# Optimization experiments

Hardware: AMD Instinct MI355X
Metric: run time of the kernel (lower is better)

## Reference

```python
import jax, jax.numpy as jnp
import numpy as np

DEPTH, FEAT, HID = 20, 2048, 1024
HALF = FEAT // 2
CLAMP = 2.0
TWO_OVER_PI = 0.6366197723675814  # FrEIA's 0.636619772


def setup_inputs() -> dict:
    key = jax.random.key(0)
    ks = jax.random.split(key, 9)
    x = jax.random.normal(ks[0], (4096, FEAT), dtype=jnp.float32)
    # FrEIA PermuteRandom: numpy permutation seeded with layer index k
    perms = jnp.asarray(
        np.stack([np.random.RandomState(k).permutation(FEAT) for k in range(DEPTH)]),
        dtype=jnp.int32,
    )
    def w(k, shape):  # module reinits all params as 0.01*randn
        return 0.01 * jax.random.normal(k, shape, dtype=jnp.float32)
    return {
        "x": x, "perms": perms,
        "s1_w1": w(ks[1], (DEPTH, HALF, HID)), "s1_b1": w(ks[2], (DEPTH, HID)),
        "s1_w2": w(ks[3], (DEPTH, HID, FEAT)), "s1_b2": w(ks[4], (DEPTH, FEAT)),
        "s2_w1": w(ks[5], (DEPTH, HALF, HID)), "s2_b1": w(ks[6], (DEPTH, HID)),
        "s2_w2": w(ks[7], (DEPTH, HID, FEAT)), "s2_b2": w(ks[8], (DEPTH, FEAT)),
    }


def _subnet(x, w1, b1, w2, b2):
    h = x @ w1 + b1
    h = jnp.where(h >= 0, h, 0.01 * h)  # LeakyReLU(negative_slope=0.01)
    return h @ w2 + b2


def reference(x, perms, s1_w1, s1_b1, s1_w2, s1_b2, s2_w1, s2_b1, s2_w2, s2_b2):
    def body(carry, xs):
        z, jac = carry
        perm, w1a, b1a, w1b, b1b, w2a, b2a, w2b, b2b = xs
        z = z[:, perm]                       # PermuteRandom
        x1, x2 = z[:, :HALF], z[:, HALF:]    # GLOW coupling split
        r2 = _subnet(x2, w2a, b2a, w2b, b2b)  # [B, FEAT] -> (s2, t2)
        e2 = CLAMP * TWO_OVER_PI * jnp.arctan(r2[:, :HALF] / CLAMP)
        y1 = jnp.exp(e2) * x1 + r2[:, HALF:]
        r1 = _subnet(y1, w1a, b1a, w1b, b1b)  # (s1, t1)
        e1 = CLAMP * TWO_OVER_PI * jnp.arctan(r1[:, :HALF] / CLAMP)
        y2 = jnp.exp(e1) * x2 + r1[:, HALF:]
        jac = jac + e1.sum(-1) + e2.sum(-1)  # log|det J| per sample
        return (jnp.concatenate([y1, y2], axis=-1), jac), None

    jac0 = jnp.zeros(x.shape[0], dtype=x.dtype)
    (z, jac), _ = jax.lax.scan(
        body, (x, jac0),
        (perms, s1_w1, s1_b1, s1_w2, s1_b2, s2_w1, s2_b1, s2_w2, s2_b2),
    )
    return z, jac
```

## Files before the change

### kernel.cpp

```cpp
#include <hip/hip_runtime.h>
#include <stdint.h>

#define DEPTH 20
#define FEAT  2048
#define HALF  1024
#define HID   1024
#define MROWS 4096

typedef __bf16 bf16x8 __attribute__((ext_vector_type(8)));
typedef float  f32x4  __attribute__((ext_vector_type(4)));
typedef unsigned int u32x4 __attribute__((ext_vector_type(4)));

__device__ __forceinline__ unsigned short f2bf(float f) {
  union { float f; unsigned int u; } v; v.f = f;
  unsigned int u = v.u + 0x7fffu + ((v.u >> 16) & 1u);
  return (unsigned short)(u >> 16);
}

__device__ __forceinline__ void async_cp16(unsigned short* lds, const unsigned short* g) {
  __builtin_amdgcn_global_load_lds(
      (const __attribute__((address_space(1))) void*)g,
      (__attribute__((address_space(3))) void*)lds, 16, 0, 0);
}

__device__ __forceinline__ bf16x8 lds_ld8(const unsigned short* p) {
  return __builtin_bit_cast(bf16x8, *(const u32x4*)p);
}

__global__ void wcvt_k(const float* __restrict__ s2w1, const float* __restrict__ s2w2,
                       const float* __restrict__ s1w1, const float* __restrict__ s1w2,
                       unsigned short* __restrict__ w2a, unsigned short* __restrict__ w2b,
                       unsigned short* __restrict__ w1a, unsigned short* __restrict__ w1b) {
  const int zid = blockIdx.z;
  const int d = zid >> 2, which = zid & 3;
  const float* src; unsigned short* dst; int N, pp;
  switch (which) {
    case 0:  src = s2w1 + (size_t)d * HALF * HID;  dst = w2a + (size_t)d * HALF * HID; N = 1024; pp = 0; break;
    case 1:  src = s2w2 + (size_t)d * HID * FEAT;  dst = w2b + (size_t)d * FEAT * HID; N = 2048; pp = 1; break;
    case 2:  src = s1w1 + (size_t)d * HALF * HID;  dst = w1a + (size_t)d * HALF * HID; N = 1024; pp = 0; break;
    default: src = s1w2 + (size_t)d * HID * FEAT;  dst = w1b + (size_t)d * FEAT * HID; N = 2048; pp = 1; break;
  }
  int nb = blockIdx.x * 32;
  if (nb >= N) return;
  int kb = blockIdx.y * 32;
  __shared__ float t[32][33];
  int tx = threadIdx.x, ty = threadIdx.y;
#pragma unroll
  for (int s = 0; s < 4; ++s)
    t[ty + 8*s][tx] = src[(size_t)(kb + ty + 8*s) * N + nb + tx];
  __syncthreads();
  int pbase = pp ? (nb < 1024 ? 2*nb : 2*(nb - 1024) + 32) : nb;
#pragma unroll
  for (int s = 0; s < 4; ++s) {
    int nl = ty + 8*s;
    dst[(size_t)(pbase + nl) * 1024 + kb + tx] = f2bf(t[tx][nl]);
  }
}

__device__ __forceinline__ int porig(int p) {
  int g = p >> 6, o = p & 63;
  return (o < 32) ? (g*32 + o) : (1024 + g*32 + (o - 32));
}

__global__ void bias_k(const float* __restrict__ s2b1, const float* __restrict__ s2b2,
                       const float* __restrict__ s1b1, const float* __restrict__ s1b2,
                       float* __restrict__ b2a, float* __restrict__ b2b,
                       float* __restrict__ b1a, float* __restrict__ b1b) {
  int i = blockIdx.x * 256 + threadIdx.x;
  if (i >= DEPTH * 6144) return;
  int d = i / 6144, j = i - d * 6144;
  if (j < 1024)      b2a[d*1024 + j] = s2b1[(size_t)d*HID + j];
  else if (j < 3072) { int p = j - 1024; b2b[d*2048 + p] = s2b2[(size_t)d*FEAT + porig(p)]; }
  else if (j < 4096) b1a[d*1024 + j - 3072] = s1b1[(size_t)d*HID + j - 3072];
  else               { int p = j - 4096; b1b[d*2048 + p] = s1b2[(size_t)d*FEAT + porig(p)]; }
}

__global__ void permute_k(const float* __restrict__ z, const int* __restrict__ perm,
                          float* __restrict__ x1f, float* __restrict__ x2f,
                          unsigned short* __restrict__ x2b) {
  int c = blockIdx.x * 256 + threadIdx.x;
  int row0 = blockIdx.y * 8;
  int pc = perm[c];
#pragma unroll
  for (int r = 0; r < 8; ++r) {
    int row = row0 + r;
    float v = z[row * FEAT + pc];
    if (c < HALF) {
      x1f[row * HALF + c] = v;
    } else {
      x2f[row * HALF + c - HALF] = v;
      x2b[row * HALF + c - HALF] = f2bf(v);
    }
  }
}

template<int EPI>
__launch_bounds__(256)
__global__ void gemm_k(const unsigned short* __restrict__ A,
                       const unsigned short* __restrict__ Bt,
                       const float* __restrict__ bias,
                       const float* __restrict__ xin,
                       float* __restrict__ yout,
                       unsigned short* __restrict__ ybf,
                       float* __restrict__ jac,
                       unsigned short* __restrict__ hout) {
  __shared__ unsigned short As[2][128 * 32];
  __shared__ unsigned short Bs[2][128 * 32];
  const int tid  = threadIdx.x;
  const int wave = tid >> 6, lane = tid & 63;
  const int quad = lane >> 4, l15 = lane & 15;
  const int wy = wave >> 1, wx = wave & 1;
  const int bm = blockIdx.y * 128;
  const int bn = blockIdx.x * 128;
  const int K = 1024;

  f32x4 acc[4][4];
#pragma unroll
  for (int i = 0; i < 4; ++i)
#pragma unroll
    for (int j = 0; j < 4; ++j)
#pragma unroll
      for (int r = 0; r < 4; ++r) acc[i][j][r] = 0.0f;

  const int gbase = wave * 64 + lane;

  auto stage = [&](int kt, int buf) {
    const int k0 = kt * 32;
#pragma unroll
    for (int i = 0; i < 2; ++i) {
      int g  = i * 256 + gbase;
      int r  = g >> 2, kg = g & 3;
      async_cp16(&As[buf][(i * 256 + wave * 64) * 8], A  + (size_t)(bm + r) * K + k0 + kg * 8);
      async_cp16(&Bs[buf][(i * 256 + wave * 64) * 8], Bt + (size_t)(bn + r) * K + k0 + kg * 8);
    }
  };

  stage(0, 0);
  __syncthreads();

  for (int kt = 0; kt < 32; ++kt) {
    const int cur = kt & 1;
    if (kt < 31) stage(kt + 1, cur ^ 1);

    bf16x8 af[4], bf[4];
#pragma unroll
    for (int i = 0; i < 4; ++i)
      af[i] = lds_ld8(&As[cur][(wy * 64 + i * 16 + l15) * 32 + quad * 8]);
#pragma unroll
    for (int j = 0; j < 4; ++j)
      bf[j] = lds_ld8(&Bs[cur][(wx * 64 + j * 16 + l15) * 32 + quad * 8]);
#pragma unroll
    for (int i = 0; i < 4; ++i)
#pragma unroll
      for (int j = 0; j < 4; ++j)
        acc[i][j] = __builtin_amdgcn_mfma_f32_16x16x32_bf16(af[i], bf[j], acc[i][j], 0, 0, 0);

    __syncthreads();
  }

  if (EPI == 0) {
    const int ldo = gridDim.x * 128;
#pragma unroll
    for (int j = 0; j < 4; ++j) {
      int col = bn + wx * 64 + j * 16 + l15;
      float bj = bias[col];
#pragma unroll
      for (int i = 0; i < 4; ++i) {
#pragma unroll
        for (int r = 0; r < 4; ++r) {
          int row = bm + wy * 64 + i * 16 + quad * 4 + r;
          float v = acc[i][j][r] + bj;
          v = v >= 0.0f ? v : 0.01f * v;
          hout[(size_t)row * ldo + col] = f2bf(v);
        }
      }
    }
  } else {
    const int g = (bn >> 6) + wx;
#pragma unroll
    for (int i = 0; i < 4; ++i) {
      float esum[4] = {0.0f, 0.0f, 0.0f, 0.0f};
#pragma unroll
      for (int j = 0; j < 2; ++j) {
        int pe = bn + wx * 64 + j * 16 + l15;
        float be = bias[pe];
        float ba = bias[pe + 32];
        int xcol = g * 32 + j * 16 + l15;
#pragma unroll
        for (int r = 0; r < 4; ++r) {
          int row = bm + wy * 64 + i * 16 + quad * 4 + r;
          float re = acc[i][j][r] + be;
          float ra = acc[i][j + 2][r] + ba;
          float e  = 1.2732395447351628f * atanf(0.5f * re);
          float y  = __expf(e) * xin[(size_t)row * HALF + xcol] + ra;
          yout[(size_t)row * FEAT + xcol] = y;
          if (ybf) ybf[(size_t)row * HALF + xcol] = f2bf(y);
          esum[r] += e;
        }
      }
#pragma unroll
      for (int r = 0; r < 4; ++r) {
        float v = esum[r];
        v += __shfl_xor(v, 1);
        v += __shfl_xor(v, 2);
        v += __shfl_xor(v, 4);
        v += __shfl_xor(v, 8);
        if (l15 == 0) {
          int row = bm + wy * 64 + i * 16 + quad * 4 + r;
          atomicAdd(&jac[row], v);
        }
      }
    }
  }
}

__global__ void jcopy_k(const float* __restrict__ jac, float* __restrict__ out) {
  int i = blockIdx.x * 256 + threadIdx.x;
  if (i < 4096) out[i] = jac[i];
}

extern "C" void kernel_launch(void* const* d_in, const int* in_sizes, int n_in,
                              void* d_out, int out_size, void* d_ws, size_t ws_size,
                              hipStream_t stream) {
  const float* x     = (const float*)d_in[0];
  const int*   perms = (const int*)d_in[1];
  const float* s1w1  = (const float*)d_in[2];
  const float* s1b1  = (const float*)d_in[3];
  const float* s1w2  = (const float*)d_in[4];
  const float* s1b2  = (const float*)d_in[5];
  const float* s2w1  = (const float*)d_in[6];
  const float* s2b1  = (const float*)d_in[7];
  const float* s2w2  = (const float*)d_in[8];
  const float* s2b2  = (const float*)d_in[9];
  float* out = (float*)d_out;

  size_t off = 0;
  char* base = (char*)d_ws;
  auto alloc = [&](size_t bytes) {
    void* r = base + off;
    off += (bytes + 255) & ~(size_t)255;
    return r;
  };
  float*          x1f = (float*)alloc((size_t)MROWS * HALF * 4);
  float*          x2f = (float*)alloc((size_t)MROWS * HALF * 4);
  unsigned short* x2b = (unsigned short*)alloc((size_t)MROWS * HALF * 2);
  unsigned short* y1b = (unsigned short*)alloc((size_t)MROWS * HALF * 2);
  unsigned short* hb  = (unsigned short*)alloc((size_t)MROWS * HID * 2);
  float*          zbuf= (float*)alloc((size_t)MROWS * FEAT * 4);
  unsigned short* w2a = (unsigned short*)alloc((size_t)DEPTH * HALF * HID * 2);
  unsigned short* w2b = (unsigned short*)alloc((size_t)DEPTH * FEAT * HID * 2);
  unsigned short* w1a = (unsigned short*)alloc((size_t)DEPTH * HALF * HID * 2);
  unsigned short* w1b = (unsigned short*)alloc((size_t)DEPTH * FEAT * HID * 2);
  float* b2a = (float*)alloc((size_t)DEPTH * 1024 * 4);
  float* b2b = (float*)alloc((size_t)DEPTH * 2048 * 4);
  float* b1a = (float*)alloc((size_t)DEPTH * 1024 * 4);
  float* b1b = (float*)alloc((size_t)DEPTH * 2048 * 4);
  float* jac = (float*)alloc(4096 * 4);

  hipMemsetAsync(jac, 0, 4096 * 4, stream);

  wcvt_k<<<dim3(64, 32, 4 * DEPTH), dim3(32, 8), 0, stream>>>(
      s2w1, s2w2, s1w1, s1w2, w2a, w2b, w1a, w1b);
  bias_k<<<(DEPTH * 6144 + 255) / 256, 256, 0, stream>>>(
      s2b1, s2b2, s1b1, s1b2, b2a, b2b, b1a, b1b);

  for (int d = 0; d < DEPTH; ++d) {
    const float* zsrc = (d == 0) ? x : zbuf;
    permute_k<<<dim3(8, 512), 256, 0, stream>>>(zsrc, perms + (size_t)d * FEAT, x1f, x2f, x2b);

    unsigned short* W2a = w2a + (size_t)d * HALF * HID;
    unsigned short* W2b = w2b + (size_t)d * FEAT * HID;
    unsigned short* W1a = w1a + (size_t)d * HALF * HID;
    unsigned short* W1b = w1b + (size_t)d * FEAT * HID;
    float* B2a = b2a + (size_t)d * 1024;
    float* B2b = b2b + (size_t)d * 2048;
    float* B1a = b1a + (size_t)d * 1024;
    float* B1b = b1b + (size_t)d * 2048;

    float* zdst = (d == DEPTH - 1) ? out : zbuf;
    gemm_k<0><<<dim3(8, 32), 256, 0, stream>>>(x2b, W2a, B2a, nullptr, nullptr, nullptr, nullptr, hb);
    gemm_k<1><<<dim3(16, 32), 256, 0, stream>>>(hb, W2b, B2b, x1f, zdst, y1b, jac, nullptr);
    gemm_k<0><<<dim3(8, 32), 256, 0, stream>>>(y1b, W1a, B1a, nullptr, nullptr, nullptr, nullptr, hb);
    gemm_k<1><<<dim3(16, 32), 256, 0, stream>>>(hb, W1b, B1b, x2f, zdst + HALF, nullptr, jac, nullptr);
  }
  jcopy_k<<<16, 256, 0, stream>>>(jac, out + (size_t)MROWS * FEAT);
}
```

Baseline: 4.355 ms.

## Shrink GEMM tile to 64x128, deepen K step to 64, add XOR-swizzled LDS

Changes the GEMM block tile from 128x128 to 64x128 and doubles the grid in M, giving twice as many workgroups on the 256-CU part. Each K step now covers 64 instead of 32. It uses a single LDS buffer with an explicit vmcnt wait instead of double buffering, and XOR-swizzles 16-byte chunks within a row to avoid LDS bank conflicts on the fragment reads. The trade-offs are lost global/compute overlap and lower reuse of B per block.

```diff
diff --git a/kernel.cpp b/kernel.cpp
--- a/kernel.cpp
+++ b/kernel.cpp
@@ -104,19 +104,19 @@
                        unsigned short* __restrict__ ybf,
                        float* __restrict__ jac,
                        unsigned short* __restrict__ hout) {
-  __shared__ unsigned short As[2][128 * 32];
-  __shared__ unsigned short Bs[2][128 * 32];
+  __shared__ unsigned short As[64 * 64];
+  __shared__ unsigned short Bs[128 * 64];
   const int tid  = threadIdx.x;
   const int wave = tid >> 6, lane = tid & 63;
   const int quad = lane >> 4, l15 = lane & 15;
   const int wy = wave >> 1, wx = wave & 1;
-  const int bm = blockIdx.y * 128;
+  const int bm = blockIdx.y * 64;
   const int bn = blockIdx.x * 128;
   const int K = 1024;
 
-  f32x4 acc[4][4];
-#pragma unroll
-  for (int i = 0; i < 4; ++i)
+  f32x4 acc[2][4];
+#pragma unroll
+  for (int i = 0; i < 2; ++i)
 #pragma unroll
     for (int j = 0; j < 4; ++j)
 #pragma unroll
@@ -124,37 +124,42 @@
 
   const int gbase = wave * 64 + lane;
 
-  auto stage = [&](int kt, int buf) {
-    const int k0 = kt * 32;
+  for (int kt = 0; kt < 16; ++kt) {
+    const int k0 = kt * 64;
 #pragma unroll
     for (int i = 0; i < 2; ++i) {
       int g  = i * 256 + gbase;
-      int r  = g >> 2, kg = g & 3;
-      async_cp16(&As[buf][(i * 256 + wave * 64) * 8], A  + (size_t)(bm + r) * K + k0 + kg * 8);
-      async_cp16(&Bs[buf][(i * 256 + wave * 64) * 8], Bt + (size_t)(bn + r) * K + k0 + kg * 8);
-    }
-  };
-
-  stage(0, 0);
-  __syncthreads();
-
-  for (int kt = 0; kt < 32; ++kt) {
-    const int cur = kt & 1;
-    if (kt < 31) stage(kt + 1, cur ^ 1);
-
-    bf16x8 af[4], bf[4];
-#pragma unroll
-    for (int i = 0; i < 4; ++i)
-      af[i] = lds_ld8(&As[cur][(wy * 64 + i * 16 + l15) * 32 + quad * 8]);
-#pragma unroll
-    for (int j = 0; j < 4; ++j)
-      bf[j] = lds_ld8(&Bs[cur][(wx * 64 + j * 16 + l15) * 32 + quad * 8]);
-#pragma unroll
-    for (int i = 0; i < 4; ++i)
-#pragma unroll
-      for (int j = 0; j < 4; ++j)
-        acc[i][j] = __builtin_amdgcn_mfma_f32_16x16x32_bf16(af[i], bf[j], acc[i][j], 0, 0, 0);
-
+      int r  = g >> 3, kg = (g & 7) ^ (r & 7);
+      async_cp16(&As[(i * 256 + wave * 64) * 8], A + (size_t)(bm + r) * K + k0 + kg * 8);
+    }
+#pragma unroll
+    for (int i = 0; i < 4; ++i) {
+      int g  = i * 256 + gbase;
+      int r  = g >> 3, kg = (g & 7) ^ (r & 7);
+      async_cp16(&Bs[(i * 256 + wave * 64) * 8], Bt + (size_t)(bn + r) * K + k0 + kg * 8);
+    }
+    asm volatile("s_waitcnt vmcnt(0)" ::: "memory");
+    __syncthreads();
+
+#pragma unroll
+    for (int kk = 0; kk < 2; ++kk) {
+      bf16x8 af[2], bf[4];
+#pragma unroll
+      for (int i = 0; i < 2; ++i) {
+        int ar = wy * 32 + i * 16 + l15;
+        af[i] = lds_ld8(&As[ar * 64 + (((kk * 4 + quad) ^ (ar & 7))) * 8]);
+      }
+#pragma unroll
+      for (int j = 0; j < 4; ++j) {
+        int br = wx * 64 + j * 16 + l15;
+        bf[j] = lds_ld8(&Bs[br * 64 + (((kk * 4 + quad) ^ (br & 7))) * 8]);
+      }
+#pragma unroll
+      for (int i = 0; i < 2; ++i)
+#pragma unroll
+        for (int j = 0; j < 4; ++j)
+          acc[i][j] = __builtin_amdgcn_mfma_f32_16x16x32_bf16(af[i], bf[j], acc[i][j], 0, 0, 0);
+    }
     __syncthreads();
   }
 
@@ -165,10 +170,10 @@
       int col = bn + wx * 64 + j * 16 + l15;
       float bj = bias[col];
 #pragma unroll
-      for (int i = 0; i < 4; ++i) {
+      for (int i = 0; i < 2; ++i) {
 #pragma unroll
         for (int r = 0; r < 4; ++r) {
-          int row = bm + wy * 64 + i * 16 + quad * 4 + r;
+          int row = bm + wy * 32 + i * 16 + quad * 4 + r;
           float v = acc[i][j][r] + bj;
           v = v >= 0.0f ? v : 0.01f * v;
           hout[(size_t)row * ldo + col] = f2bf(v);
@@ -178,7 +183,7 @@
   } else {
     const int g = (bn >> 6) + wx;
 #pragma unroll
-    for (int i = 0; i < 4; ++i) {
+    for (int i = 0; i < 2; ++i) {
       float esum[4] = {0.0f, 0.0f, 0.0f, 0.0f};
 #pragma unroll
       for (int j = 0; j < 2; ++j) {
@@ -188,7 +193,7 @@
         int xcol = g * 32 + j * 16 + l15;
 #pragma unroll
         for (int r = 0; r < 4; ++r) {
-          int row = bm + wy * 64 + i * 16 + quad * 4 + r;
+          int row = bm + wy * 32 + i * 16 + quad * 4 + r;
           float re = acc[i][j][r] + be;
           float ra = acc[i][j + 2][r] + ba;
           float e  = 1.2732395447351628f * atanf(0.5f * re);
@@ -206,7 +211,7 @@
         v += __shfl_xor(v, 4);
         v += __shfl_xor(v, 8);
         if (l15 == 0) {
-          int row = bm + wy * 64 + i * 16 + quad * 4 + r;
+          int row = bm + wy * 32 + i * 16 + quad * 4 + r;
           atomicAdd(&jac[row], v);
         }
       }
@@ -278,10 +283,10 @@
     float* B1b = b1b + (size_t)d * 2048;
 
     float* zdst = (d == DEPTH - 1) ? out : zbuf;
-    gemm_k<0><<<dim3(8, 32), 256, 0, stream>>>(x2b, W2a, B2a, nullptr, nullptr, nullptr, nullptr, hb);
-    gemm_k<1><<<dim3(16, 32), 256, 0, stream>>>(hb, W2b, B2b, x1f, zdst, y1b, jac, nullptr);
-    gemm_k<0><<<dim3(8, 32), 256, 0, stream>>>(y1b, W1a, B1a, nullptr, nullptr, nullptr, nullptr, hb);
-    gemm_k<1><<<dim3(16, 32), 256, 0, stream>>>(hb, W1b, B1b, x2f, zdst + HALF, nullptr, jac, nullptr);
+    gemm_k<0><<<dim3(8, 64), 256, 0, stream>>>(x2b, W2a, B2a, nullptr, nullptr, nullptr, nullptr, hb);
+    gemm_k<1><<<dim3(16, 64), 256, 0, stream>>>(hb, W2b, B2b, x1f, zdst, y1b, jac, nullptr);
+    gemm_k<0><<<dim3(8, 64), 256, 0, stream>>>(y1b, W1a, B1a, nullptr, nullptr, nullptr, nullptr, hb);
+    gemm_k<1><<<dim3(16, 64), 256, 0, stream>>>(hb, W1b, B1b, x2f, zdst + HALF, nullptr, jac, nullptr);
   }
   jcopy_k<<<16, 256, 0, stream>>>(jac, out + (size_t)MROWS * FEAT);
 }
```

Result: faster. 3.503 ms (-19.6%).
